# Kernel tuning notes

Measured on AMD Instinct MI355X. Metric: run time of the kernel, lower is better.

Reference implementation:

```python
import jax, jax.numpy as jnp
import numpy as np

N_FEAT = 1024
N_COMP = 512
N_HID = 256
N_CLASS = 2
N_INS = 8
N_BAG = 100000


def setup_inputs() -> dict:
    key = jax.random.key(0)
    ks = jax.random.split(key, 8)
    g = lambda k, shp, fan: jax.random.normal(k, shp, jnp.float32) * np.sqrt(2.0 / (fan[0] + fan[1]))
    return {
        "x": jax.random.normal(ks[0], (N_BAG, N_FEAT), jnp.float32),
        "slide_label": 1,  # static bag label
        # gated attention net (G_Att_Net) params
        "Wc": g(ks[1], (N_FEAT, N_COMP), (N_FEAT, N_COMP)), "bc": jnp.zeros((N_COMP,), jnp.float32),
        "W1": g(ks[2], (N_COMP, N_HID), (N_COMP, N_HID)), "b1": jnp.zeros((N_HID,), jnp.float32),
        "W2": g(ks[3], (N_COMP, N_HID), (N_COMP, N_HID)), "b2": jnp.zeros((N_HID,), jnp.float32),
        "W3": g(ks[4], (N_HID, N_CLASS), (N_HID, N_CLASS)), "b3": jnp.zeros((N_CLASS,), jnp.float32),
        # instance classifier (Ins) params
        "W_ins": g(ks[5], (N_COMP, N_CLASS), (N_COMP, N_CLASS)), "b_ins": jnp.zeros((N_CLASS,), jnp.float32),
        # bag classifier (S_Bag) params
        "W_bag": g(ks[6], (N_COMP, 1), (N_COMP, 1)), "b_bag": jnp.zeros((1,), jnp.float32),
    }


def reference(x, slide_label, Wc, bc, W1, b1, W2, b2, W3, b3, W_ins, b_ins, W_bag, b_bag):
    # --- G_Att_Net: compression + gated attention (vectorized over N instances) ---
    h = jax.nn.relu(x @ Wc + bc)                       # [N, 512]
    a = jnp.tanh(h @ W1 + b1) * jax.nn.sigmoid(h @ W2 + b2)  # [N, 256]
    att_score = a @ W3 + b3                            # [N, n_class] raw scores
    A = jax.nn.softmax(att_score, axis=-1)             # softmax over class axis (as in TF code)

    # --- Ins: top-k positive/negative instance selection for the in-bag class ---
    A_I = A[:, slide_label]                            # [N]
    _, top_pos_ids = jax.lax.top_k(A_I, N_INS)         # highest-attention instances
    _, top_neg_ids = jax.lax.top_k(-A_I, N_INS)        # lowest-attention instances
    ins_in = jnp.concatenate([h[top_pos_ids], h[top_neg_ids]], axis=0)  # [2*n_ins, 512]
    ins_logits_unnorm = ins_in @ W_ins + b_ins         # [2*n_ins, n_class]
    ins_logits = jax.nn.softmax(ins_logits_unnorm, axis=-1)
    ins_labels = jnp.concatenate([jnp.ones((N_INS,), jnp.int32), jnp.zeros((N_INS,), jnp.int32)])

    # --- S_Bag: slide-level aggregation sum_i A[i]^T h[i] = A^T h ---
    slide_agg = jnp.einsum("nc,nd->cd", A, h)          # [n_class, 512]
    slide_score_unnorm = (slide_agg @ W_bag + b_bag).reshape(1, N_CLASS)  # [1, n_class]
    Y_prob = jax.nn.softmax(slide_score_unnorm, axis=-1)
    Y_hat = jnp.argmax(slide_score_unnorm, axis=-1)

    return (att_score, A, h, ins_labels, ins_logits_unnorm, ins_logits,
            slide_score_unnorm, Y_prob, Y_hat)
```

## Files before the change

### kernel.cpp

```cpp
#include <hip/hip_runtime.h>
#include <hip/hip_bf16.h>

#define M_ROWS 100000
#define NFEAT 1024
#define NCOMP 512
#define NHID 256
#define NB 782
#define NC (NB * 8)
#define LDA 72

using bf16x8 = __attribute__((ext_vector_type(8))) __bf16;
using f32x4  = __attribute__((ext_vector_type(4))) float;

__device__ inline unsigned short f2bf(float f) {
  return __builtin_bit_cast(unsigned short, (__bf16)f);
}

__global__ void k_prep(const float* __restrict__ Wc, const float* __restrict__ W1,
                       const float* __restrict__ W2, const float* __restrict__ b3,
                       unsigned short* __restrict__ WcT, unsigned short* __restrict__ W1T,
                       unsigned short* __restrict__ W2T, float* __restrict__ slide_agg,
                       float* __restrict__ att) {
  int tid = blockIdx.x * blockDim.x + threadIdx.x;
  int stride = gridDim.x * blockDim.x;
  for (int i = tid; i < NCOMP * NFEAT; i += stride) {
    int n = i >> 10, k = i & (NFEAT - 1);
    WcT[i] = f2bf(Wc[k * NCOMP + n]);
  }
  for (int i = tid; i < NHID * NCOMP; i += stride) {
    int n = i >> 9, k = i & (NCOMP - 1);
    W1T[i] = f2bf(W1[k * NHID + n]);
    W2T[i] = f2bf(W2[k * NHID + n]);
  }
  for (int i = tid; i < 2 * NCOMP; i += stride) slide_agg[i] = 0.f;
  float b30 = b3[0], b31 = b3[1];
  for (int i = tid; i < M_ROWS; i += stride) {
    *(float2*)(att + 2 * i) = make_float2(b30, b31);
  }
}

__global__ __launch_bounds__(256, 2)
void k_gemm1(const float* __restrict__ x, const unsigned short* __restrict__ WcT,
             const float* __restrict__ bc, float* __restrict__ h) {
  __shared__ unsigned short Al[128 * LDA];
  __shared__ unsigned short Bl[128 * LDA];
  const int xcd = blockIdx.x & 7;
  const int local = blockIdx.x >> 3;
  const int nt = local & 3;
  const int mt = (local >> 2) * 8 + xcd;
  if (mt >= NB) return;
  const int m0 = mt * 128, n0 = nt * 128;
  const int t = threadIdx.x;
  const int wave = t >> 6, lane = t & 63;
  const int wm = wave & 1, wn = wave >> 1;
  const int lo = lane & 15, quad = lane >> 4;

  const int arow = t >> 4, ach = t & 15;
  const int brow = t >> 3, bch = t & 7;

  f32x4 acc[4][4] = {};
  float4 aPre[8];
  uint4  bPre[4];

  {
    #pragma unroll
    for (int i = 0; i < 8; i++) {
      int gr = m0 + arow + i * 16;
      aPre[i] = (gr < M_ROWS) ? *(const float4*)(x + (size_t)gr * NFEAT + ach * 4)
                              : make_float4(0.f, 0.f, 0.f, 0.f);
    }
    #pragma unroll
    for (int i = 0; i < 4; i++)
      bPre[i] = *(const uint4*)(WcT + (n0 + brow + i * 32) * NFEAT + bch * 8);
  }

  for (int kk = 0; kk < NFEAT; kk += 64) {
    #pragma unroll
    for (int i = 0; i < 8; i++) {
      float4 v = aPre[i];
      *(ushort4*)(&Al[(arow + i * 16) * LDA + ach * 4]) =
          make_ushort4(f2bf(v.x), f2bf(v.y), f2bf(v.z), f2bf(v.w));
    }
    #pragma unroll
    for (int i = 0; i < 4; i++)
      *(uint4*)(&Bl[(brow + i * 32) * LDA + bch * 8]) = bPre[i];
    __syncthreads();

    if (kk + 64 < NFEAT) {
      int kn = kk + 64;
      #pragma unroll
      for (int i = 0; i < 8; i++) {
        int gr = m0 + arow + i * 16;
        aPre[i] = (gr < M_ROWS) ? *(const float4*)(x + (size_t)gr * NFEAT + kn + ach * 4)
                                : make_float4(0.f, 0.f, 0.f, 0.f);
      }
      #pragma unroll
      for (int i = 0; i < 4; i++)
        bPre[i] = *(const uint4*)(WcT + (n0 + brow + i * 32) * NFEAT + kn + bch * 8);
    }

    #pragma unroll
    for (int ks = 0; ks < 2; ks++) {
      bf16x8 af[4], bfr[4];
      #pragma unroll
      for (int mf = 0; mf < 4; mf++)
        af[mf] = *(const bf16x8*)(&Al[(wm * 64 + mf * 16 + lo) * LDA + ks * 32 + quad * 8]);
      #pragma unroll
      for (int nf = 0; nf < 4; nf++)
        bfr[nf] = *(const bf16x8*)(&Bl[(wn * 64 + nf * 16 + lo) * LDA + ks * 32 + quad * 8]);
      #pragma unroll
      for (int mf = 0; mf < 4; mf++)
        #pragma unroll
        for (int nf = 0; nf < 4; nf++)
          acc[mf][nf] = __builtin_amdgcn_mfma_f32_16x16x32_bf16(af[mf], bfr[nf], acc[mf][nf], 0, 0, 0);
    }
    __syncthreads();
  }
  #pragma unroll
  for (int nf = 0; nf < 4; nf++) {
    int col = n0 + wn * 64 + nf * 16 + lo;
    float bias = bc[col];
    #pragma unroll
    for (int mf = 0; mf < 4; mf++) {
      int rb = m0 + wm * 64 + mf * 16 + quad * 4;
      #pragma unroll
      for (int r = 0; r < 4; r++) {
        int row = rb + r;
        if (row < M_ROWS) {
          float v = acc[mf][nf][r] + bias;
          h[(size_t)row * NCOMP + col] = fmaxf(v, 0.f);
        }
      }
    }
  }
}

__global__ __launch_bounds__(512, 2)
void k_gemm2(const float* __restrict__ h, const unsigned short* __restrict__ W1T,
             const unsigned short* __restrict__ W2T, const float* __restrict__ b1,
             const float* __restrict__ b2, const float* __restrict__ W3,
             float* __restrict__ att) {
  __shared__ unsigned short Al[128 * LDA];
  __shared__ unsigned short B1l[128 * LDA];
  __shared__ unsigned short B2l[128 * LDA];
  const int xcd = blockIdx.x & 7;
  const int local = blockIdx.x >> 3;
  const int nt = local & 1;
  const int mt = (local >> 1) * 8 + xcd;
  if (mt >= NB) return;
  const int m0 = mt * 128, n0 = nt * 128;
  const int t = threadIdx.x;
  const int wave = t >> 6, lane = t & 63;
  const int wm = wave & 3, wn = wave >> 2;
  const int lo = lane & 15, quad = lane >> 4;

  const int arow = t >> 4, ach = t & 15;
  const int brow = t >> 3, bch = t & 7;

  f32x4 acc1[2][4] = {};
  f32x4 acc2[2][4] = {};
  float4 aPre[4];
  uint4  b1Pre[2], b2Pre[2];

  {
    #pragma unroll
    for (int i = 0; i < 4; i++) {
      int gr = m0 + arow + i * 32;
      aPre[i] = (gr < M_ROWS) ? *(const float4*)(h + (size_t)gr * NCOMP + ach * 4)
                              : make_float4(0.f, 0.f, 0.f, 0.f);
    }
    #pragma unroll
    for (int i = 0; i < 2; i++) {
      int src = (n0 + brow + i * 64) * NCOMP + bch * 8;
      b1Pre[i] = *(const uint4*)(W1T + src);
      b2Pre[i] = *(const uint4*)(W2T + src);
    }
  }

  for (int kk = 0; kk < NCOMP; kk += 64) {
    #pragma unroll
    for (int i = 0; i < 4; i++) {
      float4 v = aPre[i];
      *(ushort4*)(&Al[(arow + i * 32) * LDA + ach * 4]) =
          make_ushort4(f2bf(v.x), f2bf(v.y), f2bf(v.z), f2bf(v.w));
    }
    #pragma unroll
    for (int i = 0; i < 2; i++) {
      *(uint4*)(&B1l[(brow + i * 64) * LDA + bch * 8]) = b1Pre[i];
      *(uint4*)(&B2l[(brow + i * 64) * LDA + bch * 8]) = b2Pre[i];
    }
    __syncthreads();

    if (kk + 64 < NCOMP) {
      int kn = kk + 64;
      #pragma unroll
      for (int i = 0; i < 4; i++) {
        int gr = m0 + arow + i * 32;
        aPre[i] = (gr < M_ROWS) ? *(const float4*)(h + (size_t)gr * NCOMP + kn + ach * 4)
                                : make_float4(0.f, 0.f, 0.f, 0.f);
      }
      #pragma unroll
      for (int i = 0; i < 2; i++) {
        int src = (n0 + brow + i * 64) * NCOMP + kn + bch * 8;
        b1Pre[i] = *(const uint4*)(W1T + src);
        b2Pre[i] = *(const uint4*)(W2T + src);
      }
    }

    #pragma unroll
    for (int ks = 0; ks < 2; ks++) {
      bf16x8 af[2], b1f[4], b2f[4];
      #pragma unroll
      for (int mf = 0; mf < 2; mf++)
        af[mf] = *(const bf16x8*)(&Al[(wm * 32 + mf * 16 + lo) * LDA + ks * 32 + quad * 8]);
      #pragma unroll
      for (int nf = 0; nf < 4; nf++) {
        b1f[nf] = *(const bf16x8*)(&B1l[(wn * 64 + nf * 16 + lo) * LDA + ks * 32 + quad * 8]);
        b2f[nf] = *(const bf16x8*)(&B2l[(wn * 64 + nf * 16 + lo) * LDA + ks * 32 + quad * 8]);
      }
      #pragma unroll
      for (int mf = 0; mf < 2; mf++)
        #pragma unroll
        for (int nf = 0; nf < 4; nf++) {
          acc1[mf][nf] = __builtin_amdgcn_mfma_f32_16x16x32_bf16(af[mf], b1f[nf], acc1[mf][nf], 0, 0, 0);
          acc2[mf][nf] = __builtin_amdgcn_mfma_f32_16x16x32_bf16(af[mf], b2f[nf], acc2[mf][nf], 0, 0, 0);
        }
    }
    __syncthreads();
  }
  float p[2][4][2] = {};
  #pragma unroll
  for (int nf = 0; nf < 4; nf++) {
    int col = n0 + wn * 64 + nf * 16 + lo;
    float bb1 = b1[col], bb2 = b2[col];
    float w30 = W3[col * 2], w31 = W3[col * 2 + 1];
    #pragma unroll
    for (int mf = 0; mf < 2; mf++)
      #pragma unroll
      for (int r = 0; r < 4; r++) {
        float g1 = acc1[mf][nf][r] + bb1;
        float g2 = acc2[mf][nf][r] + bb2;
        float e = __expf(-2.f * g1);
        float th = (1.f - e) / (1.f + e);
        float sg = 1.f / (1.f + __expf(-g2));
        float a = th * sg;
        p[mf][r][0] += a * w30;
        p[mf][r][1] += a * w31;
      }
  }
  #pragma unroll
  for (int mask = 1; mask < 16; mask <<= 1)
    #pragma unroll
    for (int mf = 0; mf < 2; mf++)
      #pragma unroll
      for (int r = 0; r < 4; r++) {
        p[mf][r][0] += __shfl_xor(p[mf][r][0], mask, 64);
        p[mf][r][1] += __shfl_xor(p[mf][r][1], mask, 64);
      }
  if (lo == 0) {
    #pragma unroll
    for (int mf = 0; mf < 2; mf++)
      #pragma unroll
      for (int r = 0; r < 4; r++) {
        int row = m0 + wm * 32 + mf * 16 + quad * 4 + r;
        if (row < M_ROWS) {
          atomicAdd(&att[row * 2],     p[mf][r][0]);
          atomicAdd(&att[row * 2 + 1], p[mf][r][1]);
        }
      }
  }
}

__global__ __launch_bounds__(256)
void k_soft(const float* __restrict__ att, const float* __restrict__ h,
            const int* __restrict__ slide_label, float* __restrict__ A,
            float* __restrict__ slide_agg, float* __restrict__ cand_val,
            int* __restrict__ cand_idx) {
  __shared__ float As[128][2];
  __shared__ float AIt[128];
  __shared__ float AIb[128];
  const int m0 = blockIdx.x * 128;
  const int t = threadIdx.x;
  const int sl = *slide_label;
  if (t < 128) {
    int r = m0 + t;
    float A0 = 0.f, A1 = 0.f;
    bool valid = (r < M_ROWS);
    if (valid) {
      float a0 = att[2 * r], a1 = att[2 * r + 1];
      float mx = fmaxf(a0, a1);
      float e0 = __expf(a0 - mx), e1 = __expf(a1 - mx);
      float s = e0 + e1;
      A0 = e0 / s; A1 = e1 / s;
      A[2 * r] = A0; A[2 * r + 1] = A1;
    }
    As[t][0] = A0; As[t][1] = A1;
    float ai = (sl == 0) ? A0 : A1;
    AIt[t] = valid ? ai : -3.4e38f;
    AIb[t] = valid ? ai : 3.4e38f;
  }
  __syncthreads();
  int nrows = min(128, M_ROWS - m0);
  float a00 = 0, a01 = 0, a10 = 0, a11 = 0;
  int d = t * 2;
  #pragma unroll 2
  for (int r = 0; r < nrows; r++) {
    float2 hv = *(const float2*)(h + (size_t)(m0 + r) * NCOMP + d);
    float A0 = As[r][0], A1 = As[r][1];
    a00 += A0 * hv.x; a01 += A0 * hv.y;
    a10 += A1 * hv.x; a11 += A1 * hv.y;
  }
  atomicAdd(&slide_agg[d], a00);
  atomicAdd(&slide_agg[d + 1], a01);
  atomicAdd(&slide_agg[NCOMP + d], a10);
  atomicAdd(&slide_agg[NCOMP + d + 1], a11);
  if (t < 64) {
    for (int it = 0; it < 8; it++) {
      float v0 = AIt[t], v1 = AIt[t + 64];
      float v = v0; int vi = t;
      if (v1 > v) { v = v1; vi = t + 64; }
      #pragma unroll
      for (int mask = 32; mask >= 1; mask >>= 1) {
        float ov = __shfl_xor(v, mask, 64);
        int oi = __shfl_xor(vi, mask, 64);
        if (ov > v || (ov == v && oi < vi)) { v = ov; vi = oi; }
      }
      if (t == 0) {
        cand_val[blockIdx.x * 16 + it] = v;
        cand_idx[blockIdx.x * 16 + it] = m0 + vi;
      }
      AIt[vi] = -3.4e38f;
    }
    for (int it = 0; it < 8; it++) {
      float v0 = AIb[t], v1 = AIb[t + 64];
      float v = v0; int vi = t;
      if (v1 < v) { v = v1; vi = t + 64; }
      #pragma unroll
      for (int mask = 32; mask >= 1; mask >>= 1) {
        float ov = __shfl_xor(v, mask, 64);
        int oi = __shfl_xor(vi, mask, 64);
        if (ov < v || (ov == v && oi < vi)) { v = ov; vi = oi; }
      }
      if (t == 0) {
        cand_val[blockIdx.x * 16 + 8 + it] = v;
        cand_idx[blockIdx.x * 16 + 8 + it] = m0 + vi;
      }
      AIb[vi] = 3.4e38f;
    }
  }
}

__global__ __launch_bounds__(256)
void k_final(const float* __restrict__ h, const float* __restrict__ W_ins,
             const float* __restrict__ b_ins, const float* __restrict__ W_bag,
             const float* __restrict__ b_bag, const float* __restrict__ slide_agg,
             const float* __restrict__ cand_val, const int* __restrict__ cand_idx,
             float* __restrict__ out_lab, float* __restrict__ out_insu,
             float* __restrict__ out_ins, float* __restrict__ out_slide,
             float* __restrict__ out_yprob, float* __restrict__ out_yhat) {
  __shared__ float tv[NC];
  __shared__ int   ti[NC];
  __shared__ float lv[256];
  __shared__ int   li[256];
  __shared__ int   lp[256];
  __shared__ int   ids[16];
  __shared__ float insu[16][2];
  __shared__ float ssc[2];
  const int t = threadIdx.x;

  for (int i = t; i < NC; i += 256) {
    int blk = i >> 3, j = i & 7;
    tv[i] = cand_val[blk * 16 + j];
    ti[i] = cand_idx[blk * 16 + j];
  }
  __syncthreads();
  for (int it = 0; it < 8; it++) {
    float bv = -3.4e38f; int bi = 0x7fffffff, bp = -1;
    for (int i = t; i < NC; i += 256) {
      float v = tv[i]; int idx = ti[i];
      if (v > bv || (v == bv && idx < bi)) { bv = v; bi = idx; bp = i; }
    }
    lv[t] = bv; li[t] = bi; lp[t] = bp;
    __syncthreads();
    for (int s = 128; s >= 1; s >>= 1) {
      if (t < s) {
        float ov = lv[t + s]; int oi = li[t + s];
        if (ov > lv[t] || (ov == lv[t] && oi < li[t])) { lv[t] = ov; li[t] = oi; lp[t] = lp[t + s]; }
      }
      __syncthreads();
    }
    if (t == 0) { ids[it] = li[0]; tv[lp[0]] = -3.4e38f; }
    __syncthreads();
  }
  for (int i = t; i < NC; i += 256) {
    int blk = i >> 3, j = i & 7;
    tv[i] = cand_val[blk * 16 + 8 + j];
    ti[i] = cand_idx[blk * 16 + 8 + j];
  }
  __syncthreads();
  for (int it = 0; it < 8; it++) {
    float bv = 3.4e38f; int bi = 0x7fffffff, bp = -1;
    for (int i = t; i < NC; i += 256) {
      float v = tv[i]; int idx = ti[i];
      if (v < bv || (v == bv && idx < bi)) { bv = v; bi = idx; bp = i; }
    }
    lv[t] = bv; li[t] = bi; lp[t] = bp;
    __syncthreads();
    for (int s = 128; s >= 1; s >>= 1) {
      if (t < s) {
        float ov = lv[t + s]; int oi = li[t + s];
        if (ov < lv[t] || (ov == lv[t] && oi < li[t])) { lv[t] = ov; li[t] = oi; lp[t] = lp[t + s]; }
      }
      __syncthreads();
    }
    if (t == 0) { ids[8 + it] = li[0]; tv[lp[0]] = 3.4e38f; }
    __syncthreads();
  }
  {
    int g = t >> 3, j = t & 7;
    int row = g >> 1, cls = g & 1;
    int id = ids[row];
    float dot = 0.f;
    for (int dd = j; dd < NCOMP; dd += 8)
      dot += h[(size_t)id * NCOMP + dd] * W_ins[dd * 2 + cls];
    #pragma unroll
    for (int mask = 1; mask < 8; mask <<= 1)
      dot += __shfl_xor(dot, mask, 64);
    if (j == 0) insu[row][cls] = dot + b_ins[cls];
  }
  __syncthreads();
  if (t < 16) {
    float u0 = insu[t][0], u1 = insu[t][1];
    out_insu[t * 2] = u0; out_insu[t * 2 + 1] = u1;
    float mx = fmaxf(u0, u1);
    float e0 = __expf(u0 - mx), e1 = __expf(u1 - mx);
    float s = e0 + e1;
    out_ins[t * 2] = e0 / s; out_ins[t * 2 + 1] = e1 / s;
    out_lab[t] = (t < 8) ? 1.0f : 0.0f;
  }
  if (t < 64) {
    int c = t >> 5, j = t & 31;
    float dot = 0.f;
    for (int dd = j; dd < NCOMP; dd += 32)
      dot += slide_agg[c * NCOMP + dd] * W_bag[dd];
    #pragma unroll
    for (int mask = 1; mask < 32; mask <<= 1)
      dot += __shfl_xor(dot, mask, 64);
    if (j == 0) ssc[c] = dot + b_bag[0];
  }
  __syncthreads();
  if (t == 0) {
    float s0 = ssc[0], s1 = ssc[1];
    out_slide[0] = s0; out_slide[1] = s1;
    float mx = fmaxf(s0, s1);
    float e0 = __expf(s0 - mx), e1 = __expf(s1 - mx);
    float s = e0 + e1;
    out_yprob[0] = e0 / s; out_yprob[1] = e1 / s;
    out_yhat[0] = (s1 > s0) ? 1.0f : 0.0f;
  }
}

extern "C" void kernel_launch(void* const* d_in, const int* in_sizes, int n_in,
                              void* d_out, int out_size, void* d_ws, size_t ws_size,
                              hipStream_t stream) {
  const float* x     = (const float*)d_in[0];
  const int*   slide = (const int*)d_in[1];
  const float* Wc    = (const float*)d_in[2];
  const float* bc    = (const float*)d_in[3];
  const float* W1    = (const float*)d_in[4];
  const float* b1    = (const float*)d_in[5];
  const float* W2    = (const float*)d_in[6];
  const float* b2    = (const float*)d_in[7];
  const float* W3    = (const float*)d_in[8];
  const float* b3    = (const float*)d_in[9];
  const float* W_ins = (const float*)d_in[10];
  const float* b_ins = (const float*)d_in[11];
  const float* W_bag = (const float*)d_in[12];
  const float* b_bag = (const float*)d_in[13];

  float* out = (float*)d_out;
  float* att     = out;
  float* A       = out + 200000;
  float* h       = out + 400000;
  float* o_lab   = out + 51600000;
  float* o_insu  = out + 51600016;
  float* o_ins   = out + 51600048;
  float* o_slide = out + 51600080;
  float* o_yprob = out + 51600082;
  float* o_yhat  = out + 51600084;

  char* ws = (char*)d_ws;
  unsigned short* WcT = (unsigned short*)(ws);
  unsigned short* W1T = (unsigned short*)(ws + 1048576);
  unsigned short* W2T = (unsigned short*)(ws + 1048576 + 262144);
  float* slide_agg = (float*)(ws + 1572864);
  float* cand_val  = (float*)(ws + 1576960);
  int*   cand_idx  = (int*)(ws + 1627008);

  k_prep<<<512, 256, 0, stream>>>(Wc, W1, W2, b3, WcT, W1T, W2T, slide_agg, att);
  k_gemm1<<<3136, 256, 0, stream>>>(x, WcT, bc, h);
  k_gemm2<<<1568, 512, 0, stream>>>(h, W1T, W2T, b1, b2, W3, att);
  k_soft<<<NB, 256, 0, stream>>>(att, h, slide, A, slide_agg, cand_val, cand_idx);
  k_final<<<1, 256, 0, stream>>>(h, W_ins, b_ins, W_bag, b_bag, slide_agg,
                                 cand_val, cand_idx, o_lab, o_insu, o_ins,
                                 o_slide, o_yprob, o_yhat);
}
```

Baseline: 1.300 ms.

## Pre-convert x and h to bf16 and stage GEMM tiles via direct global-to-LDS loads

Adds a prep pass that converts x to bf16 in workspace, and has the first GEMM also write a bf16 copy of h. Both GEMMs then load tiles with global_load_lds DMA straight into shared memory instead of loading fp32 and converting in registers. The aim is to cut per-tile conversion and register staging work. The cost is an extra full read of x plus about 300 MB of extra writes, and the path only runs if the workspace is large enough.

```diff
diff --git a/kernel.cpp b/kernel.cpp
--- a/kernel.cpp
+++ b/kernel.cpp
@@ -9,11 +9,28 @@
 #define NC (NB * 8)
 #define LDA 72
 
+#define WS_WCT   0
+#define WS_W1T   1048576
+#define WS_W2T   1310720
+#define WS_SAGG  1572864
+#define WS_CVAL  1576960
+#define WS_CIDX  1627008
+#define WS_XBF   1677312ULL
+#define WS_HBF   (WS_XBF + 204800000ULL)
+#define WS_REQ   (WS_HBF + 102400000ULL + 262144ULL)
+
 using bf16x8 = __attribute__((ext_vector_type(8))) __bf16;
 using f32x4  = __attribute__((ext_vector_type(4))) float;
 
 __device__ inline unsigned short f2bf(float f) {
   return __builtin_bit_cast(unsigned short, (__bf16)f);
+}
+
+__device__ __forceinline__ void g2l16(const void* g, void* l) {
+  __builtin_amdgcn_global_load_lds(
+      (const __attribute__((address_space(1))) unsigned int*)(unsigned long long)g,
+      (__attribute__((address_space(3))) unsigned int*)(unsigned int)(unsigned long long)l,
+      16, 0, 0);
 }
 
 __global__ void k_prep(const float* __restrict__ Wc, const float* __restrict__ W1,
@@ -36,6 +53,206 @@
   float b30 = b3[0], b31 = b3[1];
   for (int i = tid; i < M_ROWS; i += stride) {
     *(float2*)(att + 2 * i) = make_float2(b30, b31);
+  }
+}
+
+__global__ void k_prep2(const float* __restrict__ x, const float* __restrict__ Wc,
+                        const float* __restrict__ W1, const float* __restrict__ W2,
+                        const float* __restrict__ b3, unsigned short* __restrict__ xbf,
+                        unsigned short* __restrict__ WcT, unsigned short* __restrict__ W1T,
+                        unsigned short* __restrict__ W2T, float* __restrict__ slide_agg,
+                        float* __restrict__ att) {
+  int tid = blockIdx.x * blockDim.x + threadIdx.x;
+  int stride = gridDim.x * blockDim.x;
+  for (int i = tid; i < M_ROWS * NFEAT / 4; i += stride) {
+    float4 v = ((const float4*)x)[i];
+    ((ushort4*)xbf)[i] = make_ushort4(f2bf(v.x), f2bf(v.y), f2bf(v.z), f2bf(v.w));
+  }
+  for (int i = tid; i < NCOMP * NFEAT; i += stride) {
+    int n = i >> 10, k = i & (NFEAT - 1);
+    WcT[i] = f2bf(Wc[k * NCOMP + n]);
+  }
+  for (int i = tid; i < NHID * NCOMP; i += stride) {
+    int n = i >> 9, k = i & (NCOMP - 1);
+    W1T[i] = f2bf(W1[k * NHID + n]);
+    W2T[i] = f2bf(W2[k * NHID + n]);
+  }
+  for (int i = tid; i < 2 * NCOMP; i += stride) slide_agg[i] = 0.f;
+  float b30 = b3[0], b31 = b3[1];
+  for (int i = tid; i < M_ROWS; i += stride) {
+    *(float2*)(att + 2 * i) = make_float2(b30, b31);
+  }
+}
+
+__global__ __launch_bounds__(256, 2)
+void k_gemm1n(const unsigned short* __restrict__ xbf, const unsigned short* __restrict__ WcT,
+              const float* __restrict__ bc, float* __restrict__ h,
+              unsigned short* __restrict__ hbf) {
+  __shared__ unsigned short Al[128 * 64];
+  __shared__ unsigned short Bl[128 * 64];
+  const int xcd = blockIdx.x & 7;
+  const int local = blockIdx.x >> 3;
+  const int nt = local & 3;
+  const int mt = (local >> 2) * 8 + xcd;
+  if (mt >= NB) return;
+  const int m0 = mt * 128, n0 = nt * 128;
+  const int t = threadIdx.x;
+  const int wave = t >> 6, lane = t & 63;
+  const int wm = wave & 1, wn = wave >> 1;
+  const int lo = lane & 15, quad = lane >> 4;
+
+  const int srow = lane >> 3;
+  const int scol = (lane & 7) * 8;
+  const unsigned short* Ag = xbf + (size_t)(m0 + wave * 32 + srow) * NFEAT + scol;
+  const unsigned short* Bg = WcT + (size_t)(n0 + wave * 32 + srow) * NFEAT + scol;
+  unsigned short* Alw = &Al[wave * 4 * 512];
+  unsigned short* Blw = &Bl[wave * 4 * 512];
+
+  f32x4 acc[4][4] = {};
+
+  for (int kk = 0; kk < NFEAT; kk += 64) {
+    #pragma unroll
+    for (int i = 0; i < 4; i++) {
+      g2l16(Ag + (size_t)(i * 8) * NFEAT + kk, Alw + i * 512);
+      g2l16(Bg + (size_t)(i * 8) * NFEAT + kk, Blw + i * 512);
+    }
+    asm volatile("s_waitcnt vmcnt(0)" ::: "memory");
+    __syncthreads();
+    #pragma unroll
+    for (int ks = 0; ks < 2; ks++) {
+      bf16x8 af[4], bfr[4];
+      #pragma unroll
+      for (int mf = 0; mf < 4; mf++)
+        af[mf] = *(const bf16x8*)(&Al[(wm * 64 + mf * 16 + lo) * 64 + ks * 32 + quad * 8]);
+      #pragma unroll
+      for (int nf = 0; nf < 4; nf++)
+        bfr[nf] = *(const bf16x8*)(&Bl[(wn * 64 + nf * 16 + lo) * 64 + ks * 32 + quad * 8]);
+      #pragma unroll
+      for (int mf = 0; mf < 4; mf++)
+        #pragma unroll
+        for (int nf = 0; nf < 4; nf++)
+          acc[mf][nf] = __builtin_amdgcn_mfma_f32_16x16x32_bf16(af[mf], bfr[nf], acc[mf][nf], 0, 0, 0);
+    }
+    __syncthreads();
+  }
+  #pragma unroll
+  for (int nf = 0; nf < 4; nf++) {
+    int col = n0 + wn * 64 + nf * 16 + lo;
+    float bias = bc[col];
+    #pragma unroll
+    for (int mf = 0; mf < 4; mf++) {
+      int rb = m0 + wm * 64 + mf * 16 + quad * 4;
+      #pragma unroll
+      for (int r = 0; r < 4; r++) {
+        int row = rb + r;
+        if (row < M_ROWS) {
+          float v = fmaxf(acc[mf][nf][r] + bias, 0.f);
+          h[(size_t)row * NCOMP + col] = v;
+          hbf[(size_t)row * NCOMP + col] = f2bf(v);
+        }
+      }
+    }
+  }
+}
+
+__global__ __launch_bounds__(512, 2)
+void k_gemm2n(const unsigned short* __restrict__ hbf, const unsigned short* __restrict__ W1T,
+              const unsigned short* __restrict__ W2T, const float* __restrict__ b1,
+              const float* __restrict__ b2, const float* __restrict__ W3,
+              float* __restrict__ att) {
+  __shared__ unsigned short Al[128 * 64];
+  __shared__ unsigned short B1l[128 * 64];
+  __shared__ unsigned short B2l[128 * 64];
+  const int xcd = blockIdx.x & 7;
+  const int local = blockIdx.x >> 3;
+  const int nt = local & 1;
+  const int mt = (local >> 1) * 8 + xcd;
+  if (mt >= NB) return;
+  const int m0 = mt * 128, n0 = nt * 128;
+  const int t = threadIdx.x;
+  const int wave = t >> 6, lane = t & 63;
+  const int wm = wave & 3, wn = wave >> 2;
+  const int lo = lane & 15, quad = lane >> 4;
+
+  const int srow = lane >> 3;
+  const int scol = (lane & 7) * 8;
+  const unsigned short* Ag  = hbf + (size_t)(m0 + wave * 16 + srow) * NCOMP + scol;
+  const unsigned short* B1g = W1T + (size_t)(n0 + wave * 16 + srow) * NCOMP + scol;
+  const unsigned short* B2g = W2T + (size_t)(n0 + wave * 16 + srow) * NCOMP + scol;
+  unsigned short* Alw = &Al[wave * 1024];
+  unsigned short* B1w = &B1l[wave * 1024];
+  unsigned short* B2w = &B2l[wave * 1024];
+
+  f32x4 acc1[2][4] = {};
+  f32x4 acc2[2][4] = {};
+
+  for (int kk = 0; kk < NCOMP; kk += 64) {
+    #pragma unroll
+    for (int i = 0; i < 2; i++) {
+      g2l16(Ag  + (size_t)(i * 8) * NCOMP + kk, Alw + i * 512);
+      g2l16(B1g + (size_t)(i * 8) * NCOMP + kk, B1w + i * 512);
+      g2l16(B2g + (size_t)(i * 8) * NCOMP + kk, B2w + i * 512);
+    }
+    asm volatile("s_waitcnt vmcnt(0)" ::: "memory");
+    __syncthreads();
+    #pragma unroll
+    for (int ks = 0; ks < 2; ks++) {
+      bf16x8 af[2];
+      #pragma unroll
+      for (int mf = 0; mf < 2; mf++)
+        af[mf] = *(const bf16x8*)(&Al[(wm * 32 + mf * 16 + lo) * 64 + ks * 32 + quad * 8]);
+      #pragma unroll
+      for (int nf = 0; nf < 4; nf++) {
+        bf16x8 b1f = *(const bf16x8*)(&B1l[(wn * 64 + nf * 16 + lo) * 64 + ks * 32 + quad * 8]);
+        acc1[0][nf] = __builtin_amdgcn_mfma_f32_16x16x32_bf16(af[0], b1f, acc1[0][nf], 0, 0, 0);
+        acc1[1][nf] = __builtin_amdgcn_mfma_f32_16x16x32_bf16(af[1], b1f, acc1[1][nf], 0, 0, 0);
+        bf16x8 b2f = *(const bf16x8*)(&B2l[(wn * 64 + nf * 16 + lo) * 64 + ks * 32 + quad * 8]);
+        acc2[0][nf] = __builtin_amdgcn_mfma_f32_16x16x32_bf16(af[0], b2f, acc2[0][nf], 0, 0, 0);
+        acc2[1][nf] = __builtin_amdgcn_mfma_f32_16x16x32_bf16(af[1], b2f, acc2[1][nf], 0, 0, 0);
+      }
+    }
+    __syncthreads();
+  }
+  float p[2][4][2] = {};
+  #pragma unroll
+  for (int nf = 0; nf < 4; nf++) {
+    int col = n0 + wn * 64 + nf * 16 + lo;
+    float bb1 = b1[col], bb2 = b2[col];
+    float w30 = W3[col * 2], w31 = W3[col * 2 + 1];
+    #pragma unroll
+    for (int mf = 0; mf < 2; mf++)
+      #pragma unroll
+      for (int r = 0; r < 4; r++) {
+        float g1 = acc1[mf][nf][r] + bb1;
+        float g2 = acc2[mf][nf][r] + bb2;
+        float e = __expf(-2.f * g1);
+        float th = (1.f - e) / (1.f + e);
+        float sg = 1.f / (1.f + __expf(-g2));
+        float a = th * sg;
+        p[mf][r][0] += a * w30;
+        p[mf][r][1] += a * w31;
+      }
+  }
+  #pragma unroll
+  for (int mask = 1; mask < 16; mask <<= 1)
+    #pragma unroll
+    for (int mf = 0; mf < 2; mf++)
+      #pragma unroll
+      for (int r = 0; r < 4; r++) {
+        p[mf][r][0] += __shfl_xor(p[mf][r][0], mask, 64);
+        p[mf][r][1] += __shfl_xor(p[mf][r][1], mask, 64);
+      }
+  if (lo == 0) {
+    #pragma unroll
+    for (int mf = 0; mf < 2; mf++)
+      #pragma unroll
+      for (int r = 0; r < 4; r++) {
+        int row = m0 + wm * 32 + mf * 16 + quad * 4 + r;
+        if (row < M_ROWS) {
+          atomicAdd(&att[row * 2],     p[mf][r][0]);
+          atomicAdd(&att[row * 2 + 1], p[mf][r][1]);
+        }
+      }
   }
 }
 
@@ -490,16 +707,24 @@
   float* o_yhat  = out + 51600084;
 
   char* ws = (char*)d_ws;
-  unsigned short* WcT = (unsigned short*)(ws);
-  unsigned short* W1T = (unsigned short*)(ws + 1048576);
-  unsigned short* W2T = (unsigned short*)(ws + 1048576 + 262144);
-  float* slide_agg = (float*)(ws + 1572864);
-  float* cand_val  = (float*)(ws + 1576960);
-  int*   cand_idx  = (int*)(ws + 1627008);
-
-  k_prep<<<512, 256, 0, stream>>>(Wc, W1, W2, b3, WcT, W1T, W2T, slide_agg, att);
-  k_gemm1<<<3136, 256, 0, stream>>>(x, WcT, bc, h);
-  k_gemm2<<<1568, 512, 0, stream>>>(h, W1T, W2T, b1, b2, W3, att);
+  unsigned short* WcT = (unsigned short*)(ws + WS_WCT);
+  unsigned short* W1T = (unsigned short*)(ws + WS_W1T);
+  unsigned short* W2T = (unsigned short*)(ws + WS_W2T);
+  float* slide_agg = (float*)(ws + WS_SAGG);
+  float* cand_val  = (float*)(ws + WS_CVAL);
+  int*   cand_idx  = (int*)(ws + WS_CIDX);
+  unsigned short* xbf = (unsigned short*)(ws + WS_XBF);
+  unsigned short* hbf = (unsigned short*)(ws + WS_HBF);
+
+  if (ws_size >= WS_REQ) {
+    k_prep2<<<2048, 256, 0, stream>>>(x, Wc, W1, W2, b3, xbf, WcT, W1T, W2T, slide_agg, att);
+    k_gemm1n<<<3136, 256, 0, stream>>>(xbf, WcT, bc, h, hbf);
+    k_gemm2n<<<1568, 512, 0, stream>>>(hbf, W1T, W2T, b1, b2, W3, att);
+  } else {
+    k_prep<<<512, 256, 0, stream>>>(Wc, W1, W2, b3, WcT, W1T, W2T, slide_agg, att);
+    k_gemm1<<<3136, 256, 0, stream>>>(x, WcT, bc, h);
+    k_gemm2<<<1568, 512, 0, stream>>>(h, W1T, W2T, b1, b2, W3, att);
+  }
   k_soft<<<NB, 256, 0, stream>>>(att, h, slide, A, slide_agg, cand_val, cand_idx);
   k_final<<<1, 256, 0, stream>>>(h, W_ins, b_ins, W_bag, b_bag, slide_agg,
                                  cand_val, cand_idx, o_lab, o_insu, o_ins,
```

New measurement: 1.111 ms. 1.17x faster.

## Use direct global-to-LDS loads and a bf16 copy of h for downstream kernels

Applied to the files above, without the earlier changes.

Both GEMM kernels now use global_load_lds to copy tiles straight from global memory into shared memory, replacing the register-staged prefetch. The padding is removed, and gemm1 keeps x in fp32 in LDS and converts it to bf16 when loading fragments. gemm1 also writes a bf16 copy of h to workspace, which gemm2 and the softmax/aggregation kernel read instead of the fp32 h, halving their read traffic for h. In exchange, the software prefetch overlap is lost (each iteration waits on vmcnt(0)), the unpadded LDS layout may cause bank conflicts, gemm1 does extra writes, and slide_agg now uses bf16-rounded h.

```diff
diff --git a/kernel.cpp b/kernel.cpp
--- a/kernel.cpp
+++ b/kernel.cpp
@@ -7,13 +7,28 @@
 #define NHID 256
 #define NB 782
 #define NC (NB * 8)
-#define LDA 72
+
+#define WS_WCT   0
+#define WS_W1T   1048576
+#define WS_W2T   1310720
+#define WS_SAGG  1572864
+#define WS_CVAL  1576960
+#define WS_CIDX  1627008
+#define WS_HBF   1677312ULL
+#define WS_REQ   (WS_HBF + 102400000ULL + 262144ULL)
 
 using bf16x8 = __attribute__((ext_vector_type(8))) __bf16;
 using f32x4  = __attribute__((ext_vector_type(4))) float;
 
 __device__ inline unsigned short f2bf(float f) {
   return __builtin_bit_cast(unsigned short, (__bf16)f);
+}
+
+__device__ __forceinline__ void g2l16(const void* g, void* l) {
+  __builtin_amdgcn_global_load_lds(
+      (const __attribute__((address_space(1))) unsigned int*)(unsigned long long)g,
+      (__attribute__((address_space(3))) unsigned int*)(unsigned int)(unsigned long long)l,
+      16, 0, 0);
 }
 
 __global__ void k_prep(const float* __restrict__ Wc, const float* __restrict__ W1,
@@ -40,10 +55,11 @@
 }
 
 __global__ __launch_bounds__(256, 2)
-void k_gemm1(const float* __restrict__ x, const unsigned short* __restrict__ WcT,
-             const float* __restrict__ bc, float* __restrict__ h) {
-  __shared__ unsigned short Al[128 * LDA];
-  __shared__ unsigned short Bl[128 * LDA];
+void k_gemm1n(const float* __restrict__ x, const unsigned short* __restrict__ WcT,
+              const float* __restrict__ bc, float* __restrict__ h,
+              unsigned short* __restrict__ hbf) {
+  __shared__ float Af[128 * 64];
+  __shared__ unsigned short Bl[128 * 64];
   const int xcd = blockIdx.x & 7;
   const int local = blockIdx.x >> 3;
   const int nt = local & 3;
@@ -55,59 +71,45 @@
   const int wm = wave & 1, wn = wave >> 1;
   const int lo = lane & 15, quad = lane >> 4;
 
-  const int arow = t >> 4, ach = t & 15;
-  const int brow = t >> 3, bch = t & 7;
+  const int ar = lane >> 4;
+  const int ac = (lane & 15) * 4;
+  const int br = lane >> 3;
+  const int bch = (lane & 7) * 8;
+  const unsigned short* Bg = WcT + (size_t)(n0 + wave * 32 + br) * NFEAT + bch;
+  float* Afw = &Af[wave * 8 * 256];
+  unsigned short* Blw = &Bl[wave * 4 * 512];
 
   f32x4 acc[4][4] = {};
-  float4 aPre[8];
-  uint4  bPre[4];
-
-  {
+
+  for (int kk = 0; kk < NFEAT; kk += 64) {
     #pragma unroll
     for (int i = 0; i < 8; i++) {
-      int gr = m0 + arow + i * 16;
-      aPre[i] = (gr < M_ROWS) ? *(const float4*)(x + (size_t)gr * NFEAT + ach * 4)
-                              : make_float4(0.f, 0.f, 0.f, 0.f);
+      int grow = m0 + wave * 32 + i * 4 + ar;
+      if (grow > M_ROWS - 1) grow = M_ROWS - 1;
+      g2l16(x + (size_t)grow * NFEAT + kk + ac, Afw + i * 256);
     }
     #pragma unroll
     for (int i = 0; i < 4; i++)
-      bPre[i] = *(const uint4*)(WcT + (n0 + brow + i * 32) * NFEAT + bch * 8);
-  }
-
-  for (int kk = 0; kk < NFEAT; kk += 64) {
-    #pragma unroll
-    for (int i = 0; i < 8; i++) {
-      float4 v = aPre[i];
-      *(ushort4*)(&Al[(arow + i * 16) * LDA + ach * 4]) =
-          make_ushort4(f2bf(v.x), f2bf(v.y), f2bf(v.z), f2bf(v.w));
-    }
-    #pragma unroll
-    for (int i = 0; i < 4; i++)
-      *(uint4*)(&Bl[(brow + i * 32) * LDA + bch * 8]) = bPre[i];
-    __syncthreads();
-
-    if (kk + 64 < NFEAT) {
-      int kn = kk + 64;
-      #pragma unroll
-      for (int i = 0; i < 8; i++) {
-        int gr = m0 + arow + i * 16;
-        aPre[i] = (gr < M_ROWS) ? *(const float4*)(x + (size_t)gr * NFEAT + kn + ach * 4)
-                                : make_float4(0.f, 0.f, 0.f, 0.f);
-      }
-      #pragma unroll
-      for (int i = 0; i < 4; i++)
-        bPre[i] = *(const uint4*)(WcT + (n0 + brow + i * 32) * NFEAT + kn + bch * 8);
-    }
+      g2l16(Bg + (size_t)(i * 8) * NFEAT + kk, Blw + i * 512);
+    asm volatile("s_waitcnt vmcnt(0)" ::: "memory");
+    __syncthreads();
 
     #pragma unroll
     for (int ks = 0; ks < 2; ks++) {
       bf16x8 af[4], bfr[4];
       #pragma unroll
-      for (int mf = 0; mf < 4; mf++)
-        af[mf] = *(const bf16x8*)(&Al[(wm * 64 + mf * 16 + lo) * LDA + ks * 32 + quad * 8]);
+      for (int mf = 0; mf < 4; mf++) {
+        const float* ap = &Af[(wm * 64 + mf * 16 + lo) * 64 + ks * 32 + quad * 8];
+        f32x4 a0 = *(const f32x4*)ap;
+        f32x4 a1 = *(const f32x4*)(ap + 4);
+        bf16x8 v;
+        #pragma unroll
+        for (int j = 0; j < 4; j++) { v[j] = (__bf16)a0[j]; v[j + 4] = (__bf16)a1[j]; }
+        af[mf] = v;
+      }
       #pragma unroll
       for (int nf = 0; nf < 4; nf++)
-        bfr[nf] = *(const bf16x8*)(&Bl[(wn * 64 + nf * 16 + lo) * LDA + ks * 32 + quad * 8]);
+        bfr[nf] = *(const bf16x8*)(&Bl[(wn * 64 + nf * 16 + lo) * 64 + ks * 32 + quad * 8]);
       #pragma unroll
       for (int mf = 0; mf < 4; mf++)
         #pragma unroll
@@ -127,8 +129,9 @@
       for (int r = 0; r < 4; r++) {
         int row = rb + r;
         if (row < M_ROWS) {
-          float v = acc[mf][nf][r] + bias;
-          h[(size_t)row * NCOMP + col] = fmaxf(v, 0.f);
+          float v = fmaxf(acc[mf][nf][r] + bias, 0.f);
+          h[(size_t)row * NCOMP + col] = v;
+          hbf[(size_t)row * NCOMP + col] = f2bf(v);
         }
       }
     }
@@ -136,13 +139,13 @@
 }
 
 __global__ __launch_bounds__(512, 2)
-void k_gemm2(const float* __restrict__ h, const unsigned short* __restrict__ W1T,
-             const unsigned short* __restrict__ W2T, const float* __restrict__ b1,
-             const float* __restrict__ b2, const float* __restrict__ W3,
-             float* __restrict__ att) {
-  __shared__ unsigned short Al[128 * LDA];
-  __shared__ unsigned short B1l[128 * LDA];
-  __shared__ unsigned short B2l[128 * LDA];
+void k_gemm2n(const unsigned short* __restrict__ hbf, const unsigned short* __restrict__ W1T,
+              const unsigned short* __restrict__ W2T, const float* __restrict__ b1,
+              const float* __restrict__ b2, const float* __restrict__ W3,
+              float* __restrict__ att) {
+  __shared__ unsigned short Al[128 * 64];
+  __shared__ unsigned short B1l[128 * 64];
+  __shared__ unsigned short B2l[128 * 64];
   const int xcd = blockIdx.x & 7;
   const int local = blockIdx.x >> 3;
   const int nt = local & 1;
@@ -154,77 +157,42 @@
   const int wm = wave & 3, wn = wave >> 2;
   const int lo = lane & 15, quad = lane >> 4;
 
-  const int arow = t >> 4, ach = t & 15;
-  const int brow = t >> 3, bch = t & 7;
+  const int srow = lane >> 3;
+  const int scol = (lane & 7) * 8;
+  const unsigned short* Ag  = hbf + (size_t)(m0 + wave * 16 + srow) * NCOMP + scol;
+  const unsigned short* B1g = W1T + (size_t)(n0 + wave * 16 + srow) * NCOMP + scol;
+  const unsigned short* B2g = W2T + (size_t)(n0 + wave * 16 + srow) * NCOMP + scol;
+  unsigned short* Alw = &Al[wave * 1024];
+  unsigned short* B1w = &B1l[wave * 1024];
+  unsigned short* B2w = &B2l[wave * 1024];
 
   f32x4 acc1[2][4] = {};
   f32x4 acc2[2][4] = {};
-  float4 aPre[4];
-  uint4  b1Pre[2], b2Pre[2];
-
-  {
-    #pragma unroll
-    for (int i = 0; i < 4; i++) {
-      int gr = m0 + arow + i * 32;
-      aPre[i] = (gr < M_ROWS) ? *(const float4*)(h + (size_t)gr * NCOMP + ach * 4)
-                              : make_float4(0.f, 0.f, 0.f, 0.f);
-    }
+
+  for (int kk = 0; kk < NCOMP; kk += 64) {
     #pragma unroll
     for (int i = 0; i < 2; i++) {
-      int src = (n0 + brow + i * 64) * NCOMP + bch * 8;
-      b1Pre[i] = *(const uint4*)(W1T + src);
-      b2Pre[i] = *(const uint4*)(W2T + src);
-    }
-  }
-
-  for (int kk = 0; kk < NCOMP; kk += 64) {
-    #pragma unroll
-    for (int i = 0; i < 4; i++) {
-      float4 v = aPre[i];
-      *(ushort4*)(&Al[(arow + i * 32) * LDA + ach * 4]) =
-          make_ushort4(f2bf(v.x), f2bf(v.y), f2bf(v.z), f2bf(v.w));
-    }
-    #pragma unroll
-    for (int i = 0; i < 2; i++) {
-      *(uint4*)(&B1l[(brow + i * 64) * LDA + bch * 8]) = b1Pre[i];
-      *(uint4*)(&B2l[(brow + i * 64) * LDA + bch * 8]) = b2Pre[i];
-    }
-    __syncthreads();
-
-    if (kk + 64 < NCOMP) {
-      int kn = kk + 64;
-      #pragma unroll
-      for (int i = 0; i < 4; i++) {
-        int gr = m0 + arow + i * 32;
-        aPre[i] = (gr < M_ROWS) ? *(const float4*)(h + (size_t)gr * NCOMP + kn + ach * 4)
-                                : make_float4(0.f, 0.f, 0.f, 0.f);
-      }
-      #pragma unroll
-      for (int i = 0; i < 2; i++) {
-        int src = (n0 + brow + i * 64) * NCOMP + kn + bch * 8;
-        b1Pre[i] = *(const uint4*)(W1T + src);
-        b2Pre[i] = *(const uint4*)(W2T + src);
-      }
-    }
-
+      g2l16(Ag  + (size_t)(i * 8) * NCOMP + kk, Alw + i * 512);
+      g2l16(B1g + (size_t)(i * 8) * NCOMP + kk, B1w + i * 512);
+      g2l16(B2g + (size_t)(i * 8) * NCOMP + kk, B2w + i * 512);
+    }
+    asm volatile("s_waitcnt vmcnt(0)" ::: "memory");
+    __syncthreads();
     #pragma unroll
     for (int ks = 0; ks < 2; ks++) {
-      bf16x8 af[2], b1f[4], b2f[4];
+      bf16x8 af[2];
       #pragma unroll
       for (int mf = 0; mf < 2; mf++)
-        af[mf] = *(const bf16x8*)(&Al[(wm * 32 + mf * 16 + lo) * LDA + ks * 32 + quad * 8]);
+        af[mf] = *(const bf16x8*)(&Al[(wm * 32 + mf * 16 + lo) * 64 + ks * 32 + quad * 8]);
       #pragma unroll
       for (int nf = 0; nf < 4; nf++) {
-        b1f[nf] = *(const bf16x8*)(&B1l[(wn * 64 + nf * 16 + lo) * LDA + ks * 32 + quad * 8]);
-        b2f[nf] = *(const bf16x8*)(&B2l[(wn * 64 + nf * 16 + lo) * LDA + ks * 32 + quad * 8]);
-      }
-      #pragma unroll
-      for (int mf = 0; mf < 2; mf++)
-        #pragma unroll
-        for (int nf = 0; nf < 4; nf++) {
-          acc1[mf][nf] = __builtin_amdgcn_mfma_f32_16x16x32_bf16(af[mf], b1f[nf], acc1[mf][nf], 0, 0, 0);
-          acc2[mf][nf] = __builtin_amdgcn_mfma_f32_16x16x32_bf16(af[mf], b2f[nf], acc2[mf][nf], 0, 0, 0);
-        }
+        bf16x8 b1f = *(const bf16x8*)(&B1l[(wn * 64 + nf * 16 + lo) * 64 + ks * 32 + quad * 8]);
+        acc1[0][nf] = __builtin_amdgcn_mfma_f32_16x16x32_bf16(af[0], b1f, acc1[0][nf], 0, 0, 0);
+        acc1[1][nf] = __builtin_amdgcn_mfma_f32_16x16x32_bf16(af[1], b1f, acc1[1][nf], 0, 0, 0);
+        bf16x8 b2f = *(const bf16x8*)(&B2l[(wn * 64 + nf * 16 + lo) * 64 + ks * 32 + quad * 8]);
+        acc2[0][nf] = __builtin_amdgcn_mfma_f32_16x16x32_bf16(af[0], b2f, acc2[0][nf], 0, 0, 0);
+        acc2[1][nf] = __builtin_amdgcn_mfma_f32_16x16x32_bf16(af[1], b2f, acc2[1][nf], 0, 0, 0);
+      }
     }
     __syncthreads();
   }
@@ -272,7 +240,7 @@
 }
 
 __global__ __launch_bounds__(256)
-void k_soft(const float* __restrict__ att, const float* __restrict__ h,
+void k_soft(const float* __restrict__ att, const unsigned short* __restrict__ hbf,
             const int* __restrict__ slide_label, float* __restrict__ A,
             float* __restrict__ slide_agg, float* __restrict__ cand_val,
             int* __restrict__ cand_idx) {
@@ -305,10 +273,12 @@
   int d = t * 2;
   #pragma unroll 2
   for (int r = 0; r < nrows; r++) {
-    float2 hv = *(const float2*)(h + (size_t)(m0 + r) * NCOMP + d);
+    unsigned int u = *(const unsigned int*)(hbf + (size_t)(m0 + r) * NCOMP + d);
+    float hx = __uint_as_float((u & 0xffffu) << 16);
+    float hy = __uint_as_float(u & 0xffff0000u);
     float A0 = As[r][0], A1 = As[r][1];
-    a00 += A0 * hv.x; a01 += A0 * hv.y;
-    a10 += A1 * hv.x; a11 += A1 * hv.y;
+    a00 += A0 * hx; a01 += A0 * hy;
+    a10 += A1 * hx; a11 += A1 * hy;
   }
   atomicAdd(&slide_agg[d], a00);
   atomicAdd(&slide_agg[d + 1], a01);
@@ -490,17 +460,18 @@
   float* o_yhat  = out + 51600084;
 
   char* ws = (char*)d_ws;
-  unsigned short* WcT = (unsigned short*)(ws);
-  unsigned short* W1T = (unsigned short*)(ws + 1048576);
-  unsigned short* W2T = (unsigned short*)(ws + 1048576 + 262144);
-  float* slide_agg = (float*)(ws + 1572864);
-  float* cand_val  = (float*)(ws + 1576960);
-  int*   cand_idx  = (int*)(ws + 1627008);
+  unsigned short* WcT = (unsigned short*)(ws + WS_WCT);
+  unsigned short* W1T = (unsigned short*)(ws + WS_W1T);
+  unsigned short* W2T = (unsigned short*)(ws + WS_W2T);
+  float* slide_agg = (float*)(ws + WS_SAGG);
+  float* cand_val  = (float*)(ws + WS_CVAL);
+  int*   cand_idx  = (int*)(ws + WS_CIDX);
+  unsigned short* hbf = (unsigned short*)(ws + WS_HBF);
 
   k_prep<<<512, 256, 0, stream>>>(Wc, W1, W2, b3, WcT, W1T, W2T, slide_agg, att);
-  k_gemm1<<<3136, 256, 0, stream>>>(x, WcT, bc, h);
-  k_gemm2<<<1568, 512, 0, stream>>>(h, W1T, W2T, b1, b2, W3, att);
-  k_soft<<<NB, 256, 0, stream>>>(att, h, slide, A, slide_agg, cand_val, cand_idx);
+  k_gemm1n<<<3136, 256, 0, stream>>>(x, WcT, bc, h, hbf);
+  k_gemm2n<<<1568, 512, 0, stream>>>(hbf, W1T, W2T, b1, b2, W3, att);
+  k_soft<<<NB, 256, 0, stream>>>(att, hbf, slide, A, slide_agg, cand_val, cand_idx);
   k_final<<<1, 256, 0, stream>>>(h, W_ins, b_ins, W_bag, b_bag, slide_agg,
                                  cand_val, cand_idx, o_lab, o_insu, o_ins,
                                  o_slide, o_yprob, o_yhat);
```

After: 1.068 ms. -17.8%, faster.
